# Kernel optimization log

Measured on AMD Instinct MI355X. Metric: run time of the kernel, lower is better.

The kernel has to match this reference:

```python
import jax, jax.numpy as jnp
import numpy as np

D = 128
HIDDEN = 512
N = 2048


def setup_inputs() -> dict:
    key = jax.random.key(0)
    k_x, k0, k1, k2 = jax.random.split(key, 4)
    x = jax.random.normal(k_x, (N, D), dtype=jnp.float32)
    # LocallyConnected init: uniform(-sqrt(1/in), sqrt(1/in))
    b0 = 1.0 / np.sqrt(D)
    b1 = 1.0 / np.sqrt(HIDDEN)
    W0 = jax.random.uniform(k0, (D, D, HIDDEN), jnp.float32, -b0, b0)
    W1 = jax.random.uniform(k1, (D, HIDDEN, HIDDEN), jnp.float32, -b1, b1)
    W2 = jax.random.uniform(k2, (D, HIDDEN, 1), jnp.float32, -b1, b1)
    return {"x": x, "W0": W0, "W1": W1, "W2": W2}


def reference(x, W0, W1, W2):
    n, d = x.shape
    # masking layer: matmul with diag(mask[i]) == elementwise zero-out of diagonal
    mask = 1.0 - jnp.eye(d, dtype=x.dtype)          # [d, d]
    h = x[:, None, :] * mask[None, :, :]            # [n, d, d]
    # per-node locally-connected MLP
    h = jax.nn.leaky_relu(jnp.einsum('ndi,dio->ndo', h, W0))   # [n, d, hidden]
    h = jax.nn.leaky_relu(jnp.einsum('ndi,dio->ndo', h, W1))   # [n, d, hidden]
    h = jnp.einsum('ndi,dio->ndo', h, W2)                      # [n, d, 1]
    return h.squeeze(-1)                                       # [n, d]
```

## Files before the change

kernel.cpp:

```cpp
#include <hip/hip_runtime.h>

#define DD 128
#define HH 512
#define NN 2048
#define NT 128
#define PLD 516

typedef __bf16 bf16x8 __attribute__((ext_vector_type(8)));
typedef __bf16 bf16x4 __attribute__((ext_vector_type(4)));
typedef float  floatx4 __attribute__((ext_vector_type(4)));

__global__ void cvt_x(const float* __restrict__ x, __bf16* __restrict__ xb) {
    int t = blockIdx.x * blockDim.x + threadIdx.x;
    float4 v = *(const float4*)(x + (size_t)t * 4);
    bf16x4 o;
    o[0] = (__bf16)v.x; o[1] = (__bf16)v.y; o[2] = (__bf16)v.z; o[3] = (__bf16)v.w;
    *(bf16x4*)(xb + (size_t)t * 4) = o;
}

__global__ void pack_w(const float* __restrict__ W, __bf16* __restrict__ Wp, int nks) {
    __shared__ __bf16 Ls[32 * PLD];
    const int d  = blockIdx.x / nks;
    const int ks = blockIdx.x % nks;
    const int tid = threadIdx.x;
    const float* src = W + ((size_t)(d * nks + ks) * 32) * HH;

#pragma unroll
    for (int it = 0; it < 16; ++it) {
        int e = (it * 256 + tid) * 4;
        float4 v = *(const float4*)(src + e);
        bf16x4 o;
        o[0] = (__bf16)v.x; o[1] = (__bf16)v.y; o[2] = (__bf16)v.z; o[3] = (__bf16)v.w;
        *(bf16x4*)(Ls + (e >> 9) * PLD + (e & 511)) = o;
    }
    __syncthreads();

#pragma unroll
    for (int it = 0; it < 8; ++it) {
        int ch = it * 256 + tid;
        int c  = ch & 15;
        int q  = (ch >> 4) & 3;
        int ct = ch >> 6;
        bf16x8 v;
#pragma unroll
        for (int j = 0; j < 8; ++j)
            v[j] = Ls[(q * 8 + j) * PLD + ct * 16 + c];
        *(bf16x8*)(Wp + ((size_t)(d * 32 + ct) * nks + ks) * 512 + (ch & 63) * 8) = v;
    }
}

__launch_bounds__(512, 2)
__global__ void grandag_main(const __bf16* __restrict__ xb,
                             const __bf16* __restrict__ W0p,
                             const __bf16* __restrict__ W1p,
                             const float* __restrict__ W2,
                             float* __restrict__ out) {
    __shared__ __bf16 h1s[NT * HH];
    __shared__ float  outp2[8][NT];

    const int b  = blockIdx.x;
    const int d  = ((b >> 7) << 3) | (b & 7);
    const int n0 = ((b >> 3) & 15) * NT;

    const int tid = threadIdx.x;
    const int w   = tid >> 6;
    const int l   = tid & 63;
    const int lc  = l & 15;
    const int lq  = l >> 4;
    const int sw  = lc & 7;
    const int lane16 = lq * 16 + lc;

    const int ksz = d >> 5;
    const int lqz = (d >> 3) & 3;
    const int jz  = d & 7;

    {
        floatx4 acc[4][8] = {};
        const __bf16* W0b = W0p + ((size_t)(d * 32 + w * 4) * 4) * 512 + (size_t)lane16 * 8;
        const __bf16* xbb = xb + (size_t)(n0 + lc) * DD + lq * 8;
#pragma unroll
        for (int ks = 0; ks < 4; ks++) {
            bf16x8 wf[4];
#pragma unroll
            for (int mt = 0; mt < 4; mt++)
                wf[mt] = *(const bf16x8*)(W0b + (size_t)(mt * 4 + ks) * 512);
            const bool domask = (ks == ksz) && (lq == lqz);
#pragma unroll
            for (int nt = 0; nt < 8; nt++) {
                bf16x8 xf = *(const bf16x8*)(xbb + (size_t)(16 * nt) * DD + ks * 32);
                if (domask) {
#pragma unroll
                    for (int j = 0; j < 8; j++)
                        if (j == jz) xf[j] = (__bf16)0.f;
                }
#pragma unroll
                for (int mt = 0; mt < 4; mt++)
                    acc[mt][nt] = __builtin_amdgcn_mfma_f32_16x16x32_bf16(
                        wf[mt], xf, acc[mt][nt], 0, 0, 0);
            }
        }
#pragma unroll
        for (int mt = 0; mt < 4; mt++) {
            const int chunk = 8 * w + 2 * mt + (lq >> 1);
#pragma unroll
            for (int nt = 0; nt < 8; nt++) {
                bf16x4 o;
#pragma unroll
                for (int g = 0; g < 4; g++) {
                    float v = acc[mt][nt][g];
                    o[g] = (__bf16)fmaxf(v, 0.01f * v);
                }
                *(bf16x4*)(h1s + (16 * nt + lc) * HH + ((chunk ^ sw) << 3) + ((lq & 1) << 2)) = o;
            }
        }
    }
    __syncthreads();

    floatx4 acc2[4][8] = {};
    {
        const __bf16* W1b = W1p + ((size_t)(d * 32 + w * 4) * 16) * 512 + (size_t)lane16 * 8;
        const __bf16* h1b = h1s + lc * HH;
#pragma unroll 4
        for (int ks = 0; ks < 16; ks++) {
            bf16x8 wf[4];
#pragma unroll
            for (int mt = 0; mt < 4; mt++)
                wf[mt] = *(const bf16x8*)(W1b + (size_t)(mt * 16 + ks) * 512);
            const int hoff = ((4 * ks + lq) ^ sw) << 3;
#pragma unroll
            for (int nt = 0; nt < 8; nt++) {
                bf16x8 hf = *(const bf16x8*)(h1b + 16 * nt * HH + hoff);
#pragma unroll
                for (int mt = 0; mt < 4; mt++)
                    acc2[mt][nt] = __builtin_amdgcn_mfma_f32_16x16x32_bf16(
                        wf[mt], hf, acc2[mt][nt], 0, 0, 0);
            }
        }
    }

    {
        const float* W2b = W2 + (size_t)d * HH + w * 64 + lq * 4;
        floatx4 w2q[4];
#pragma unroll
        for (int mt = 0; mt < 4; mt++)
            w2q[mt] = *(const floatx4*)(W2b + mt * 16);
#pragma unroll
        for (int nt = 0; nt < 8; nt++) {
            float s = 0.f;
#pragma unroll
            for (int mt = 0; mt < 4; mt++) {
#pragma unroll
                for (int g = 0; g < 4; g++) {
                    float v = acc2[mt][nt][g];
                    s += fmaxf(v, 0.01f * v) * w2q[mt][g];
                }
            }
            s += __shfl_xor(s, 16, 64);
            s += __shfl_xor(s, 32, 64);
            if (l < 16) outp2[w][16 * nt + lc] = s;
        }
    }
    __syncthreads();
    if (tid < NT) {
        float v = 0.f;
#pragma unroll
        for (int ww = 0; ww < 8; ww++) v += outp2[ww][tid];
        out[(size_t)(n0 + tid) * DD + d] = v;
    }
}

extern "C" void kernel_launch(void* const* d_in, const int* in_sizes, int n_in,
                              void* d_out, int out_size, void* d_ws, size_t ws_size,
                              hipStream_t stream) {
    const float* x  = (const float*)d_in[0];
    const float* W0 = (const float*)d_in[1];
    const float* W1 = (const float*)d_in[2];
    const float* W2 = (const float*)d_in[3];
    float* out = (float*)d_out;

    __bf16* W0p = (__bf16*)d_ws;
    __bf16* W1p = (__bf16*)((char*)d_ws + (size_t)DD * DD * HH * 2);
    __bf16* xb  = (__bf16*)((char*)d_ws + (size_t)DD * DD * HH * 2
                                        + (size_t)DD * HH * HH * 2);

    cvt_x<<<dim3(NN * DD / (256 * 4)), 256, 0, stream>>>(x, xb);
    pack_w<<<dim3(DD * (DD / 32)), 256, 0, stream>>>(W0, W0p, DD / 32);
    pack_w<<<dim3(DD * (HH / 32)), 256, 0, stream>>>(W1, W1p, HH / 32);

    grandag_main<<<dim3(DD * (NN / NT)), 512, 0, stream>>>(xb, W0p, W1p, W2, out);
}
```

Measured before the change: 420.4 us.

## Halve row tile, raise occupancy, and prefetch next weight fragments with MFMA priority

Shrinks the per-block row tile from 128 to 64, doubling the grid and halving the accumulator arrays and LDS staging, and raises launch bounds to allow three blocks per CU. Weight fragments for the next k-step are software-prefetched into registers while the current MFMAs run. The MFMA bursts are wrapped in s_setprio, and the wave index is made scalar via readfirstlane. The trade-off is that each weight fragment is now reused over half as many rows, so global weight traffic per output doubles.

```diff
diff --git a/kernel.cpp b/kernel.cpp
--- a/kernel.cpp
+++ b/kernel.cpp
@@ -3,7 +3,7 @@
 #define DD 128
 #define HH 512
 #define NN 2048
-#define NT 128
+#define NT 64
 #define PLD 516
 
 typedef __bf16 bf16x8 __attribute__((ext_vector_type(8)));
@@ -49,7 +49,7 @@
     }
 }
 
-__launch_bounds__(512, 2)
+__launch_bounds__(512, 3)
 __global__ void grandag_main(const __bf16* __restrict__ xb,
                              const __bf16* __restrict__ W0p,
                              const __bf16* __restrict__ W1p,
@@ -59,11 +59,11 @@
     __shared__ float  outp2[8][NT];
 
     const int b  = blockIdx.x;
-    const int d  = ((b >> 7) << 3) | (b & 7);
-    const int n0 = ((b >> 3) & 15) * NT;
+    const int d  = ((b >> 8) << 3) | (b & 7);
+    const int n0 = ((b >> 3) & 31) * NT;
 
     const int tid = threadIdx.x;
-    const int w   = tid >> 6;
+    const int w   = __builtin_amdgcn_readfirstlane(tid >> 6);
     const int l   = tid & 63;
     const int lc  = l & 15;
     const int lq  = l >> 4;
@@ -75,35 +75,46 @@
     const int jz  = d & 7;
 
     {
-        floatx4 acc[4][8] = {};
+        floatx4 acc[4][4] = {};
         const __bf16* W0b = W0p + ((size_t)(d * 32 + w * 4) * 4) * 512 + (size_t)lane16 * 8;
         const __bf16* xbb = xb + (size_t)(n0 + lc) * DD + lq * 8;
+        bf16x8 wf[4], wfn[4];
+#pragma unroll
+        for (int mt = 0; mt < 4; mt++)
+            wf[mt] = *(const bf16x8*)(W0b + (size_t)(mt * 4) * 512);
 #pragma unroll
         for (int ks = 0; ks < 4; ks++) {
-            bf16x8 wf[4];
+            const int ksn = (ks + 1) & 3;
 #pragma unroll
             for (int mt = 0; mt < 4; mt++)
-                wf[mt] = *(const bf16x8*)(W0b + (size_t)(mt * 4 + ks) * 512);
-            const bool domask = (ks == ksz) && (lq == lqz);
-#pragma unroll
-            for (int nt = 0; nt < 8; nt++) {
-                bf16x8 xf = *(const bf16x8*)(xbb + (size_t)(16 * nt) * DD + ks * 32);
-                if (domask) {
+                wfn[mt] = *(const bf16x8*)(W0b + (size_t)(mt * 4 + ksn) * 512);
+            bf16x8 xf[4];
+#pragma unroll
+            for (int nt = 0; nt < 4; nt++)
+                xf[nt] = *(const bf16x8*)(xbb + (size_t)(16 * nt) * DD + ks * 32);
+            if ((ks == ksz) && (lq == lqz)) {
+#pragma unroll
+                for (int nt = 0; nt < 4; nt++)
 #pragma unroll
                     for (int j = 0; j < 8; j++)
-                        if (j == jz) xf[j] = (__bf16)0.f;
-                }
+                        if (j == jz) xf[nt][j] = (__bf16)0.f;
+            }
+            __builtin_amdgcn_s_setprio(1);
+#pragma unroll
+            for (int nt = 0; nt < 4; nt++)
 #pragma unroll
                 for (int mt = 0; mt < 4; mt++)
                     acc[mt][nt] = __builtin_amdgcn_mfma_f32_16x16x32_bf16(
-                        wf[mt], xf, acc[mt][nt], 0, 0, 0);
-            }
+                        wf[mt], xf[nt], acc[mt][nt], 0, 0, 0);
+            __builtin_amdgcn_s_setprio(0);
+#pragma unroll
+            for (int mt = 0; mt < 4; mt++) wf[mt] = wfn[mt];
         }
 #pragma unroll
         for (int mt = 0; mt < 4; mt++) {
             const int chunk = 8 * w + 2 * mt + (lq >> 1);
 #pragma unroll
-            for (int nt = 0; nt < 8; nt++) {
+            for (int nt = 0; nt < 4; nt++) {
                 bf16x4 o;
 #pragma unroll
                 for (int g = 0; g < 4; g++) {
@@ -116,25 +127,35 @@
     }
     __syncthreads();
 
-    floatx4 acc2[4][8] = {};
+    floatx4 acc2[4][4] = {};
     {
         const __bf16* W1b = W1p + ((size_t)(d * 32 + w * 4) * 16) * 512 + (size_t)lane16 * 8;
         const __bf16* h1b = h1s + lc * HH;
+        bf16x8 wf[4], wfn[4];
+#pragma unroll
+        for (int mt = 0; mt < 4; mt++)
+            wf[mt] = *(const bf16x8*)(W1b + (size_t)(mt * 16) * 512);
 #pragma unroll 4
         for (int ks = 0; ks < 16; ks++) {
-            bf16x8 wf[4];
+            const int ksn = (ks + 1) & 15;
 #pragma unroll
             for (int mt = 0; mt < 4; mt++)
-                wf[mt] = *(const bf16x8*)(W1b + (size_t)(mt * 16 + ks) * 512);
+                wfn[mt] = *(const bf16x8*)(W1b + (size_t)(mt * 16 + ksn) * 512);
             const int hoff = ((4 * ks + lq) ^ sw) << 3;
-#pragma unroll
-            for (int nt = 0; nt < 8; nt++) {
-                bf16x8 hf = *(const bf16x8*)(h1b + 16 * nt * HH + hoff);
+            bf16x8 hf[4];
+#pragma unroll
+            for (int nt = 0; nt < 4; nt++)
+                hf[nt] = *(const bf16x8*)(h1b + 16 * nt * HH + hoff);
+            __builtin_amdgcn_s_setprio(1);
+#pragma unroll
+            for (int nt = 0; nt < 4; nt++)
 #pragma unroll
                 for (int mt = 0; mt < 4; mt++)
                     acc2[mt][nt] = __builtin_amdgcn_mfma_f32_16x16x32_bf16(
-                        wf[mt], hf, acc2[mt][nt], 0, 0, 0);
-            }
+                        wf[mt], hf[nt], acc2[mt][nt], 0, 0, 0);
+            __builtin_amdgcn_s_setprio(0);
+#pragma unroll
+            for (int mt = 0; mt < 4; mt++) wf[mt] = wfn[mt];
         }
     }
 
@@ -145,7 +166,7 @@
         for (int mt = 0; mt < 4; mt++)
             w2q[mt] = *(const floatx4*)(W2b + mt * 16);
 #pragma unroll
-        for (int nt = 0; nt < 8; nt++) {
+        for (int nt = 0; nt < 4; nt++) {
             float s = 0.f;
 #pragma unroll
             for (int mt = 0; mt < 4; mt++) {
```

Result: no change. 428.4 us (+1.9%).
